# Kernel optimization log

Measured on AMD Instinct MI355X. Metric: run time of the kernel, lower is better.

The kernel has to match this reference:

```python
import jax, jax.numpy as jnp
import numpy as np

B, S, E, H, V, G = 32, 2048, 300, 256, 50000, 5


def setup_inputs() -> dict:
    key = jax.random.key(0)
    ks = jax.random.split(key, 12)
    return {
        "token_ids": jax.random.randint(ks[0], (B, S), 0, V),
        "emb": jax.random.normal(ks[1], (V, E), jnp.float32) * 0.1,
        "W_ih_f": jax.random.normal(ks[2], (H, E), jnp.float32) * 0.05,
        "W_hh_f": jax.random.normal(ks[3], (H, H), jnp.float32) * 0.05,
        "b_ih_f": jax.random.normal(ks[4], (H,), jnp.float32) * 0.05,
        "b_hh_f": jax.random.normal(ks[5], (H,), jnp.float32) * 0.05,
        "W_ih_b": jax.random.normal(ks[6], (H, E), jnp.float32) * 0.05,
        "W_hh_b": jax.random.normal(ks[7], (H, H), jnp.float32) * 0.05,
        "b_ih_b": jax.random.normal(ks[8], (H,), jnp.float32) * 0.05,
        "b_hh_b": jax.random.normal(ks[9], (H,), jnp.float32) * 0.05,
        "fc_W": jax.random.normal(ks[10], (G, 2 * H), jnp.float32) * 0.05,
        "fc_b": jax.random.normal(ks[11], (G,), jnp.float32) * 0.05,
    }


def _rnn_dir(x_tm, W_ih, W_hh, b_ih, b_hh):
    # x_tm: [S, B, E] time-major. Precompute input projection once (GEMM),
    # then scan only the recurrent part. h_t = tanh(x W_ih^T + b_ih + h W_hh^T + b_hh)
    xproj = jnp.einsum('sbe,he->sbh', x_tm, W_ih) + b_ih + b_hh  # [S,B,H]
    h0 = jnp.zeros((x_tm.shape[1], W_hh.shape[0]), x_tm.dtype)

    def step(h, xp):
        h_new = jnp.tanh(xp + h @ W_hh.T)
        return h_new, h_new

    _, hs = jax.lax.scan(step, h0, xproj)
    return hs  # [S, B, H]


def reference(token_ids, emb, W_ih_f, W_hh_f, b_ih_f, b_hh_f,
              W_ih_b, W_hh_b, b_ih_b, b_hh_b, fc_W, fc_b):
    x = emb[token_ids]                      # [B, S, E] embedding lookup
    x_tm = jnp.swapaxes(x, 0, 1)            # [S, B, E]
    hs_f = _rnn_dir(x_tm, W_ih_f, W_hh_f, b_ih_f, b_hh_f)          # forward dir
    hs_b = _rnn_dir(x_tm[::-1], W_ih_b, W_hh_b, b_ih_b, b_hh_b)[::-1]  # backward dir
    out_seq = jnp.concatenate([hs_f, hs_b], axis=-1)  # [S, B, 2H]
    # MoT_layer: mean over time (vectorized form of the nested-loop mean)
    pooled = jnp.mean(out_seq, axis=0)      # [B, 2H]
    # dropout (eval / identity), then activation, then fc
    act = jnp.tanh(pooled)
    return act @ fc_W.T + fc_b              # [B, G]
```

## Files before the change

### kernel.cpp

```cpp
#include <hip/hip_runtime.h>
#include <hip/hip_bf16.h>

#define S_LEN 2048
#define BB 32
#define EE 300
#define HH 256
#define VV 50000
#define GG 5

#define K2LOG2E 2.8853900817779268f

typedef float f32x4 __attribute__((ext_vector_type(4)));
typedef __bf16 bf16x8 __attribute__((ext_vector_type(8)));
typedef int i32x4 __attribute__((ext_vector_type(4)));

__device__ __forceinline__ unsigned short f2bf(float f) {
    unsigned int u = __builtin_bit_cast(unsigned int, f);
    u = u + 0x7fffu + ((u >> 16) & 1u);
    return (unsigned short)(u >> 16);
}
__device__ __forceinline__ float bflo(unsigned int w) {
    return __builtin_bit_cast(float, w << 16);
}
__device__ __forceinline__ float bfhi(unsigned int w) {
    return __builtin_bit_cast(float, w & 0xffff0000u);
}
__device__ __forceinline__ float tanh_pre(float xs) {
    float e = __builtin_amdgcn_exp2f(xs);
    float r = __builtin_amdgcn_rcpf(e + 1.0f);
    return __builtin_fmaf(-2.0f, r, 1.0f);
}
__device__ __forceinline__ float tanhf_fast(float x) {
    return tanh_pre(x * K2LOG2E);
}
__device__ __forceinline__ unsigned int cvt_pk_bf16(float lo, float hi) {
    unsigned int r;
    asm("v_cvt_pk_bf16_f32 %0, %1, %2" : "=v"(r) : "v"(lo), "v"(hi));
    return r;
}

__global__ void k_pack(const float* __restrict__ Wih_f, const float* __restrict__ Whh_f,
                       const float* __restrict__ bih_f, const float* __restrict__ bhh_f,
                       const float* __restrict__ Wih_b, const float* __restrict__ Whh_b,
                       const float* __restrict__ bih_b, const float* __restrict__ bhh_b,
                       unsigned short* __restrict__ Wp, unsigned short* __restrict__ Whp,
                       float* __restrict__ biasc)
{
    int idx = blockIdx.x * 256 + threadIdx.x;
    if (idx < 163840) {
        int i = idx & 7, j = (idx >> 3) & 255, kg = (idx >> 11) & 3, kbd = idx >> 13;
        int kb = kbd % 10, dir = kbd / 10;
        int e = kb * 32 + kg * 8 + i;
        const float* W = dir ? Wih_b : Wih_f;
        float v = (e < EE) ? W[j * EE + e] * K2LOG2E : 0.0f;
        Wp[idx] = f2bf(v);
    } else if (idx < 163840 + 131072) {
        int x = idx - 163840;
        int i = x & 7, j = (x >> 3) & 255, kg = (x >> 11) & 3, kbd = x >> 13;
        int kb = kbd & 7, dir = kbd >> 3;
        int k = kb * 32 + kg * 8 + i;
        const float* W = dir ? Whh_b : Whh_f;
        Whp[x] = f2bf(W[j * HH + k] * K2LOG2E);
    } else if (idx < 163840 + 131072 + 512) {
        int x = idx - (163840 + 131072);
        int j = x & 255, dir = x >> 8;
        biasc[x] = (dir ? (bih_b[j] + bhh_b[j]) : (bih_f[j] + bhh_f[j])) * K2LOG2E;
    }
}

__global__ __launch_bounds__(1024) void k_xproj(
    const int* __restrict__ tok, const float* __restrict__ emb,
    const unsigned short* __restrict__ Wp, const float* __restrict__ biasc,
    unsigned short* __restrict__ xq)
{
    __shared__ char xs[32 * 640];
    int s = blockIdx.x;
    int tid = threadIdx.x;
    int lane = tid & 63, W16 = tid >> 6;

    #pragma unroll
    for (int k = 0; k < 5; k++) ((int*)xs)[tid + k * 1024] = 0;
    __syncthreads();

    {
        int b0 = W16 * 2;
        for (int rr = 0; rr < 2; rr++) {
            int b = b0 + rr;
            int t = tok[b * S_LEN + s];
            const float* row = emb + (size_t)t * EE;
            int xorv = (b & 7) << 4;
            #pragma unroll
            for (int c = 0; c < 5; c++) {
                int e = c * 64 + lane;
                if (e < EE) {
                    *(unsigned short*)(xs + b * 640 + ((2 * e) ^ xorv)) = f2bf(row[e]);
                }
            }
        }
    }
    __syncthreads();

    int dir = W16 >> 3, w = (W16 >> 1) & 3, half = W16 & 1;
    int l15 = lane & 15, kg = lane >> 4;
    f32x4 acc[4] = {};
    int brow = half * 16 + l15;
    int bxor = (brow & 7) << 4;
    const char* xrow = xs + brow * 640;

    #pragma unroll
    for (int kb = 0; kb < 10; kb++) {
        bf16x8 xb = *(const bf16x8*)(xrow + ((kb * 64 + kg * 16) ^ bxor));
        #pragma unroll
        for (int t = 0; t < 4; t++) {
            int j = w * 64 + t * 16 + l15;
            bf16x8 wa = *(const bf16x8*)(Wp + (size_t)(((dir * 10 + kb) * 4 + kg) * 256 + j) * 8);
            acc[t] = __builtin_amdgcn_mfma_f32_16x16x32_bf16(wa, xb, acc[t], 0, 0, 0);
        }
    }

    unsigned int words[8];
    #pragma unroll
    for (int t = 0; t < 4; t++) {
        float v[4];
        #pragma unroll
        for (int r = 0; r < 4; r++) {
            int j = w * 64 + t * 16 + kg * 4 + r;
            v[r] = acc[t][r] + biasc[dir * 256 + j];
        }
        words[t * 2 + 0] = cvt_pk_bf16(v[0], v[1]);
        words[t * 2 + 1] = cvt_pk_bf16(v[2], v[3]);
    }
    size_t base = (size_t)s * 32768 + (size_t)((dir * 2 + half) * 4 + w) * 2048 + (size_t)lane * 32;
    *(i32x4*)((char*)xq + base) = *(i32x4*)&words[0];
    *(i32x4*)((char*)xq + base + 16) = *(i32x4*)&words[4];
}

__global__ __launch_bounds__(1024, 4) void k_rnn(
    const unsigned short* __restrict__ xq,
    const unsigned short* __restrict__ Whp,
    float* __restrict__ pooled)
{
    __shared__ char hb0[8192];
    __shared__ char hb1[8192];
    int bid = blockIdx.x;
    int dir = bid >> 1, half = bid & 1;
    int tid = threadIdx.x;
    int lane = tid & 63, w = tid >> 6;
    int l15 = lane & 15, kg = lane >> 4;

    bf16x8 wf[8];
    #pragma unroll
    for (int kb = 0; kb < 8; kb++) {
        int j = w * 16 + l15;
        wf[kb] = *(const bf16x8*)(Whp + (size_t)(((dir * 8 + kb) * 4 + kg) * 256 + j) * 8);
    }

    *(uint2*)(&hb0[tid * 8]) = make_uint2(0, 0);

    f32x4 pool = {};

    int rbase = kg * 256 + l15 * 16;
    int woff = (w >> 1) * 1024 + ((w & 1) * 2 + (kg >> 1)) * 256 + l15 * 16 + (kg & 1) * 8;

    int lanebase = ((dir * 2 + half) * 4 + (w >> 2)) * 2048 + lane * 32 + (w & 3) * 8;
    int sdelta = dir ? -32768 : 32768;
    int s0 = dir ? (S_LEN - 1) : 0;

    const char* xqb = (const char*)xq;
    int xoff = s0 * 32768 + lanebase;
    uint2 xc0 = *(const uint2*)(xqb + xoff); xoff += sdelta;
    uint2 xc1 = *(const uint2*)(xqb + xoff); xoff += sdelta;

    __syncthreads();

#define STEP(RB, WB, XC, DO_PF)                                                      \
    {                                                                                \
        const char* rb = (RB) + rbase;                                               \
        bf16x8 hf[8];                                                                \
        _Pragma("unroll")                                                            \
        for (int kb = 0; kb < 8; kb++)                                               \
            hf[kb] = *(const bf16x8*)(rb + kb * 1024);                               \
        f32x4 acc;                                                                   \
        acc[0] = bflo(XC.x);                                                         \
        acc[1] = bfhi(XC.x);                                                         \
        acc[2] = bflo(XC.y);                                                         \
        acc[3] = bfhi(XC.y);                                                         \
        if (DO_PF) { XC = *(const uint2*)(xqb + xoff); xoff += sdelta; }             \
        _Pragma("unroll")                                                            \
        for (int kb = 0; kb < 8; kb++)                                               \
            acc = __builtin_amdgcn_mfma_f32_16x16x32_bf16(wf[kb], hf[kb],            \
                                                          acc, 0, 0, 0);             \
        float h0 = tanh_pre(acc[0]);                                                 \
        float h1 = tanh_pre(acc[1]);                                                 \
        float h2 = tanh_pre(acc[2]);                                                 \
        float h3 = tanh_pre(acc[3]);                                                 \
        unsigned int lo = cvt_pk_bf16(h0, h1);                                       \
        unsigned int hi = cvt_pk_bf16(h2, h3);                                       \
        *(uint2*)((WB) + woff) = make_uint2(lo, hi);                                 \
        asm volatile("s_waitcnt lgkmcnt(0)" ::: "memory");                           \
        __builtin_amdgcn_s_barrier();                                                \
        pool[0] += h0; pool[1] += h1; pool[2] += h2; pool[3] += h3;                  \
    }

    for (int i = 0; i < S_LEN - 4; i += 2) {
        STEP(hb0, hb1, xc0, 1)
        STEP(hb1, hb0, xc1, 1)
    }
    STEP(hb0, hb1, xc0, 1)
    STEP(hb1, hb0, xc1, 1)
    STEP(hb0, hb1, xc0, 0)
    STEP(hb1, hb0, xc1, 0)
#undef STEP

    #pragma unroll
    for (int r = 0; r < 4; r++) {
        int j = w * 16 + kg * 4 + r;
        int b = half * 16 + l15;
        pooled[b * 512 + dir * 256 + j] = pool[r];
    }
}

__global__ __launch_bounds__(64) void k_head(
    const float* __restrict__ pooled, const float* __restrict__ fcW,
    const float* __restrict__ fcb, float* __restrict__ out)
{
    int b = blockIdx.x;
    int lane = threadIdx.x;
    float p[GG] = {0, 0, 0, 0, 0};
    for (int jj = lane; jj < 512; jj += 64) {
        float a = tanhf_fast(pooled[b * 512 + jj] * (1.0f / 2048.0f));
        #pragma unroll
        for (int g = 0; g < GG; g++) p[g] += a * fcW[g * 512 + jj];
    }
    #pragma unroll
    for (int g = 0; g < GG; g++)
        #pragma unroll
        for (int off = 32; off; off >>= 1) p[g] += __shfl_xor(p[g], off);
    if (lane == 0) {
        #pragma unroll
        for (int g = 0; g < GG; g++) out[b * GG + g] = p[g] + fcb[g];
    }
}

extern "C" void kernel_launch(void* const* d_in, const int* in_sizes, int n_in,
                              void* d_out, int out_size, void* d_ws, size_t ws_size,
                              hipStream_t stream)
{
    const int* tok = (const int*)d_in[0];
    const float* emb = (const float*)d_in[1];
    const float* Wih_f = (const float*)d_in[2];
    const float* Whh_f = (const float*)d_in[3];
    const float* bih_f = (const float*)d_in[4];
    const float* bhh_f = (const float*)d_in[5];
    const float* Wih_b = (const float*)d_in[6];
    const float* Whh_b = (const float*)d_in[7];
    const float* bih_b = (const float*)d_in[8];
    const float* bhh_b = (const float*)d_in[9];
    const float* fcW = (const float*)d_in[10];
    const float* fcb = (const float*)d_in[11];
    float* out = (float*)d_out;

    char* ws = (char*)d_ws;
    unsigned short* xq   = (unsigned short*)(ws);
    unsigned short* Wp   = (unsigned short*)(ws + 67108864);
    unsigned short* Whp  = (unsigned short*)(ws + 67108864 + 327680);
    float* biasc         = (float*)(ws + 67108864 + 327680 + 262144);
    float* pooled        = (float*)(ws + 67108864 + 327680 + 262144 + 2048);

    hipLaunchKernelGGL(k_pack, dim3(1154), dim3(256), 0, stream,
                       Wih_f, Whh_f, bih_f, bhh_f, Wih_b, Whh_b, bih_b, bhh_b,
                       Wp, Whp, biasc);
    hipLaunchKernelGGL(k_xproj, dim3(2048), dim3(1024), 0, stream,
                       tok, emb, Wp, biasc, xq);
    hipLaunchKernelGGL(k_rnn, dim3(4), dim3(1024), 0, stream, xq, Whp, pooled);
    hipLaunchKernelGGL(k_head, dim3(32), dim3(64), 0, stream, pooled, fcW, fcb, out);
}
```

Before: 1.037 ms.

## Halve RNN block to 8 waves, each computing two 16-row output tiles

The recurrent kernel now runs 512 threads (8 waves) per block instead of 1024, and each wave computes two 16x16 MFMA output tiles with interleaved independent accumulators. Fewer waves take part in the per-step barrier and the two accumulator chains give some MFMA ILP within a wave. The pooled sum now uses packed f32 adds. The cost is twice the register footprint for weights and accumulators per wave, and more serial work per wave on every step.

```diff
diff --git a/kernel.cpp b/kernel.cpp
--- a/kernel.cpp
+++ b/kernel.cpp
@@ -11,6 +11,7 @@
 #define K2LOG2E 2.8853900817779268f
 
 typedef float f32x4 __attribute__((ext_vector_type(4)));
+typedef float f32x2 __attribute__((ext_vector_type(2)));
 typedef __bf16 bf16x8 __attribute__((ext_vector_type(8)));
 typedef int i32x4 __attribute__((ext_vector_type(4)));
 
@@ -37,6 +38,11 @@
     unsigned int r;
     asm("v_cvt_pk_bf16_f32 %0, %1, %2" : "=v"(r) : "v"(lo), "v"(hi));
     return r;
+}
+__device__ __forceinline__ f32x2 pk_add(f32x2 a, f32x2 b) {
+    f32x2 d;
+    asm("v_pk_add_f32 %0, %1, %2" : "=v"(d) : "v"(a), "v"(b));
+    return d;
 }
 
 __global__ void k_pack(const float* __restrict__ Wih_f, const float* __restrict__ Whh_f,
@@ -135,7 +141,7 @@
     *(i32x4*)((char*)xq + base + 16) = *(i32x4*)&words[4];
 }
 
-__global__ __launch_bounds__(1024, 4) void k_rnn(
+__global__ __launch_bounds__(512, 2) void k_rnn(
     const unsigned short* __restrict__ xq,
     const unsigned short* __restrict__ Whp,
     float* __restrict__ pooled)
@@ -148,28 +154,30 @@
     int lane = tid & 63, w = tid >> 6;
     int l15 = lane & 15, kg = lane >> 4;
 
-    bf16x8 wf[8];
+    bf16x8 wf0[8], wf1[8];
     #pragma unroll
     for (int kb = 0; kb < 8; kb++) {
-        int j = w * 16 + l15;
-        wf[kb] = *(const bf16x8*)(Whp + (size_t)(((dir * 8 + kb) * 4 + kg) * 256 + j) * 8);
-    }
-
-    *(uint2*)(&hb0[tid * 8]) = make_uint2(0, 0);
-
-    f32x4 pool = {};
+        int jbase = (((dir * 8 + kb) * 4 + kg) * 256 + w * 32 + l15);
+        wf0[kb] = *(const bf16x8*)(Whp + (size_t)jbase * 8);
+        wf1[kb] = *(const bf16x8*)(Whp + (size_t)(jbase + 16) * 8);
+    }
+
+    *(i32x4*)(&hb0[tid * 16]) = i32x4{0, 0, 0, 0};
+
+    f32x2 px[4] = {};
 
     int rbase = kg * 256 + l15 * 16;
-    int woff = (w >> 1) * 1024 + ((w & 1) * 2 + (kg >> 1)) * 256 + l15 * 16 + (kg & 1) * 8;
-
-    int lanebase = ((dir * 2 + half) * 4 + (w >> 2)) * 2048 + lane * 32 + (w & 3) * 8;
+    int woff0 = w * 1024 + (kg >> 1) * 256 + l15 * 16 + (kg & 1) * 8;
+    int woff1 = woff0 + 512;
+
+    int lanebase = ((dir * 2 + half) * 4 + (w >> 1)) * 2048 + lane * 32 + (w & 1) * 16;
     int sdelta = dir ? -32768 : 32768;
     int s0 = dir ? (S_LEN - 1) : 0;
 
     const char* xqb = (const char*)xq;
     int xoff = s0 * 32768 + lanebase;
-    uint2 xc0 = *(const uint2*)(xqb + xoff); xoff += sdelta;
-    uint2 xc1 = *(const uint2*)(xqb + xoff); xoff += sdelta;
+    i32x4 xc0 = *(const i32x4*)(xqb + xoff); xoff += sdelta;
+    i32x4 xc1 = *(const i32x4*)(xqb + xoff); xoff += sdelta;
 
     __syncthreads();
 
@@ -180,26 +188,41 @@
         _Pragma("unroll")                                                            \
         for (int kb = 0; kb < 8; kb++)                                               \
             hf[kb] = *(const bf16x8*)(rb + kb * 1024);                               \
-        f32x4 acc;                                                                   \
-        acc[0] = bflo(XC.x);                                                         \
-        acc[1] = bfhi(XC.x);                                                         \
-        acc[2] = bflo(XC.y);                                                         \
-        acc[3] = bfhi(XC.y);                                                         \
-        if (DO_PF) { XC = *(const uint2*)(xqb + xoff); xoff += sdelta; }             \
+        f32x4 acc0, acc1;                                                            \
+        acc0[0] = bflo((unsigned int)XC[0]);                                         \
+        acc0[1] = bfhi((unsigned int)XC[0]);                                         \
+        acc0[2] = bflo((unsigned int)XC[1]);                                         \
+        acc0[3] = bfhi((unsigned int)XC[1]);                                         \
+        acc1[0] = bflo((unsigned int)XC[2]);                                         \
+        acc1[1] = bfhi((unsigned int)XC[2]);                                         \
+        acc1[2] = bflo((unsigned int)XC[3]);                                         \
+        acc1[3] = bfhi((unsigned int)XC[3]);                                         \
+        if (DO_PF) { XC = *(const i32x4*)(xqb + xoff); xoff += sdelta; }             \
         _Pragma("unroll")                                                            \
-        for (int kb = 0; kb < 8; kb++)                                               \
-            acc = __builtin_amdgcn_mfma_f32_16x16x32_bf16(wf[kb], hf[kb],            \
-                                                          acc, 0, 0, 0);             \
-        float h0 = tanh_pre(acc[0]);                                                 \
-        float h1 = tanh_pre(acc[1]);                                                 \
-        float h2 = tanh_pre(acc[2]);                                                 \
-        float h3 = tanh_pre(acc[3]);                                                 \
-        unsigned int lo = cvt_pk_bf16(h0, h1);                                       \
-        unsigned int hi = cvt_pk_bf16(h2, h3);                                       \
-        *(uint2*)((WB) + woff) = make_uint2(lo, hi);                                 \
+        for (int kb = 0; kb < 8; kb++) {                                             \
+            acc0 = __builtin_amdgcn_mfma_f32_16x16x32_bf16(wf0[kb], hf[kb],          \
+                                                           acc0, 0, 0, 0);           \
+            acc1 = __builtin_amdgcn_mfma_f32_16x16x32_bf16(wf1[kb], hf[kb],          \
+                                                           acc1, 0, 0, 0);           \
+        }                                                                            \
+        float h0 = tanh_pre(acc0[0]);                                                \
+        float h1 = tanh_pre(acc0[1]);                                                \
+        float h2 = tanh_pre(acc0[2]);                                                \
+        float h3 = tanh_pre(acc0[3]);                                                \
+        float h4 = tanh_pre(acc1[0]);                                                \
+        float h5 = tanh_pre(acc1[1]);                                                \
+        float h6 = tanh_pre(acc1[2]);                                                \
+        float h7 = tanh_pre(acc1[3]);                                                \
+        *(uint2*)((WB) + woff0) = make_uint2(cvt_pk_bf16(h0, h1),                    \
+                                             cvt_pk_bf16(h2, h3));                   \
+        *(uint2*)((WB) + woff1) = make_uint2(cvt_pk_bf16(h4, h5),                    \
+                                             cvt_pk_bf16(h6, h7));                   \
         asm volatile("s_waitcnt lgkmcnt(0)" ::: "memory");                           \
         __builtin_amdgcn_s_barrier();                                                \
-        pool[0] += h0; pool[1] += h1; pool[2] += h2; pool[3] += h3;                  \
+        px[0] = pk_add(px[0], f32x2{h0, h1});                                        \
+        px[1] = pk_add(px[1], f32x2{h2, h3});                                        \
+        px[2] = pk_add(px[2], f32x2{h4, h5});                                        \
+        px[3] = pk_add(px[3], f32x2{h6, h7});                                        \
     }
 
     for (int i = 0; i < S_LEN - 4; i += 2) {
@@ -213,11 +236,13 @@
 #undef STEP
 
     #pragma unroll
-    for (int r = 0; r < 4; r++) {
-        int j = w * 16 + kg * 4 + r;
-        int b = half * 16 + l15;
-        pooled[b * 512 + dir * 256 + j] = pool[r];
-    }
+    for (int q = 0; q < 2; q++)
+        #pragma unroll
+        for (int r = 0; r < 4; r++) {
+            int j = w * 32 + q * 16 + kg * 4 + r;
+            int b = half * 16 + l15;
+            pooled[b * 512 + dir * 256 + j] = px[q * 2 + (r >> 1)][r & 1];
+        }
 }
 
 __global__ __launch_bounds__(64) void k_head(
@@ -272,6 +297,6 @@
                        Wp, Whp, biasc);
     hipLaunchKernelGGL(k_xproj, dim3(2048), dim3(1024), 0, stream,
                        tok, emb, Wp, biasc, xq);
-    hipLaunchKernelGGL(k_rnn, dim3(4), dim3(1024), 0, stream, xq, Whp, pooled);
+    hipLaunchKernelGGL(k_rnn, dim3(4), dim3(512), 0, stream, xq, Whp, pooled);
     hipLaunchKernelGGL(k_head, dim3(32), dim3(64), 0, stream, pooled, fcW, fcb, out);
 }
```

Result: slower. 1.158 ms (+11.6%).
